# Kernel optimization log

Measured on AMD Instinct MI355X. Metric: run time of the kernel, lower is better.

The kernel has to match this reference:

```python
import jax, jax.numpy as jnp
import numpy as np

B, N, M = 2, 2048, 2048
D = 1024          # query_dim == context_dim == inner_dim
H, DH = 16, 64    # heads, dim_head
SCALE = DH ** -0.5


def setup_inputs() -> dict:
    key = jax.random.key(0)
    ks = jax.random.split(key, 7)
    s = 0.02
    return {
        "x": jax.random.normal(ks[0], (B, N, D), jnp.float32),
        "context": jax.random.normal(ks[1], (B, M, D), jnp.float32),
        "Wq": jax.random.normal(ks[2], (D, H * DH), jnp.float32) * s,
        "Wk": jax.random.normal(ks[3], (D, H * DH), jnp.float32) * s,
        "Wv": jax.random.normal(ks[4], (D, H * DH), jnp.float32) * s,
        "Wo": jax.random.normal(ks[5], (H * DH, D), jnp.float32) * s,
        "bo": jax.random.normal(ks[6], (D,), jnp.float32) * s,
    }


def reference(x, context, Wq, Wk, Wv, Wo, bo):
    # Linear projections (bias-free, as in to_q/to_k/to_v)
    q = (x @ Wq).reshape(B, N, H, DH)        # [B,N,H,DH]
    k = (context @ Wk).reshape(B, M, H, DH)  # [B,M,H,DH]
    v = (context @ Wv).reshape(B, M, H, DH)
    # QK^T * scale, softmax over keys, then AV
    sim = jnp.einsum('bnhd,bmhd->bhnm', q, k) * SCALE  # [B,H,N,M]
    attn = jax.nn.softmax(sim, axis=-1)
    out = jnp.einsum('bhnm,bmhd->bnhd', attn, v)       # [B,N,H,DH]
    out = out.reshape(B, N, H * DH)
    return out @ Wo + bo  # to_out Linear; dropout=0 is identity
```

## Files before the change

kernel.cpp:

```cpp
#include <hip/hip_runtime.h>

#define B_  2
#define N_  2048
#define M_  2048
#define D_  1024
#define H_  16
#define DH_ 64

typedef __bf16 bf16x8 __attribute__((ext_vector_type(8)));
typedef __bf16 bf16x4 __attribute__((ext_vector_type(4)));
typedef short  short4v __attribute__((ext_vector_type(4)));
typedef float  f32x4  __attribute__((ext_vector_type(4)));

#define GAS(p) ((__attribute__((address_space(1))) void*)(p))
#define LAS(p) ((__attribute__((address_space(3))) void*)(p))

#define QPRESCALE 0.18033688011112042f

__device__ __forceinline__ unsigned short f2bf(float f) {
    unsigned int u = __builtin_bit_cast(unsigned int, f);
    u += 0x7fffu + ((u >> 16) & 1u);
    return (unsigned short)(u >> 16);
}

__global__ __launch_bounds__(256) void prep(
    const float* __restrict__ x, const float* __restrict__ ctx,
    const float* __restrict__ Wq, const float* __restrict__ Wk,
    const float* __restrict__ Wv, const float* __restrict__ Wo,
    unsigned short* __restrict__ xb, unsigned short* __restrict__ cb,
    unsigned short* __restrict__ WTbase)
{
    if (blockIdx.z == 4) {
        int blk = blockIdx.y * 32 + blockIdx.x;
        int stride = 1024 * 256;
        for (int i = blk * 256 + threadIdx.x; i < 2097152; i += stride) {
            const float4* src; unsigned short* dst; int j;
            if (i < 1048576) { src = (const float4*)x;   dst = xb; j = i; }
            else             { src = (const float4*)ctx; dst = cb; j = i - 1048576; }
            float4 v = src[j];
            ushort4 o = make_ushort4(f2bf(v.x), f2bf(v.y), f2bf(v.z), f2bf(v.w));
            *(ushort4*)(dst + 4*j) = o;
        }
        return;
    }
    const float* W = (blockIdx.z == 0) ? Wq : (blockIdx.z == 1) ? Wk
                    : (blockIdx.z == 2) ? Wv : Wo;
    unsigned short* WT = WTbase + (size_t)blockIdx.z * 1048576;
    __shared__ unsigned short t[32][33];
    int tx = threadIdx.x & 31, ty8 = threadIdx.x >> 5;
    int c = blockIdx.x * 32 + tx;
#pragma unroll
    for (int i = 0; i < 4; ++i) {
        int r = blockIdx.y * 32 + i*8 + ty8;
        t[i*8 + ty8][tx] = f2bf(W[(size_t)r * 1024 + c]);
    }
    __syncthreads();
    int c2 = blockIdx.y * 32 + tx;
#pragma unroll
    for (int i = 0; i < 4; ++i) {
        int r2 = blockIdx.x * 32 + i*8 + ty8;
        WT[(size_t)r2 * 1024 + c2] = t[tx][i*8 + ty8];
    }
}

__global__ __launch_bounds__(256) void gemm128(
    const unsigned short* __restrict__ xb,
    const unsigned short* __restrict__ cb,
    const unsigned short* __restrict__ wT,
    const unsigned short* __restrict__ aoA,
    unsigned short* __restrict__ qkv_out,
    const float* __restrict__ bo,
    float* __restrict__ outF,
    int base_mode)
{
    __shared__ __align__(16) unsigned short As[128*32];
    __shared__ __align__(16) unsigned short Bs[128*32];

    const int mode = base_mode + blockIdx.z;
    const unsigned short* Amat;
    const unsigned short* Bt;
    if (mode == 0)      { Amat = wT;               Bt = xb; }
    else if (mode == 1) { Amat = wT + 1048576;     Bt = cb; }
    else if (mode == 2) { Amat = cb;               Bt = wT + 2*1048576; }
    else                { Amat = wT + 3*1048576;   Bt = aoA; }

    const int tid = threadIdx.x;
    const int w = tid >> 6, l = tid & 63;
    const int quad = l >> 4, l16 = l & 15;
    const int wm = w & 1, wn = w >> 1;
    int row0, col0;
    if (mode == 2) { row0 = blockIdx.x * 128; col0 = blockIdx.y * 128; }
    else           { row0 = blockIdx.y * 128; col0 = blockIdx.x * 128; }

    f32x4 acc[4][4];
#pragma unroll
    for (int i = 0; i < 4; ++i)
#pragma unroll
        for (int j = 0; j < 4; ++j) acc[i][j] = (f32x4){0.f, 0.f, 0.f, 0.f};

    for (int k0 = 0; k0 < 1024; k0 += 32) {
        __syncthreads();
#pragma unroll
        for (int i = 0; i < 2; ++i) {
            int s = i*256 + w*64 + l;
            int m = s >> 2, c = s & 3;
            int cs = c ^ ((m >> 1) & 3);
            __builtin_amdgcn_global_load_lds(
                GAS(Amat + (size_t)(row0 + m)*1024 + k0 + cs*8),
                LAS(As + (i*256 + w*64)*8), 16, 0, 0);
            __builtin_amdgcn_global_load_lds(
                GAS(Bt + (size_t)(col0 + m)*1024 + k0 + cs*8),
                LAS(Bs + (i*256 + w*64)*8), 16, 0, 0);
        }
        __syncthreads();

        bf16x8 af[4], bfr[4];
#pragma unroll
        for (int mt = 0; mt < 4; ++mt) {
            int m = wm*64 + mt*16 + l16;
            af[mt] = *reinterpret_cast<const bf16x8*>(As + m*32 + (quad ^ ((m >> 1) & 3))*8);
            int n = wn*64 + mt*16 + l16;
            bfr[mt] = *reinterpret_cast<const bf16x8*>(Bs + n*32 + (quad ^ ((n >> 1) & 3))*8);
        }
#pragma unroll
        for (int mt = 0; mt < 4; ++mt)
#pragma unroll
            for (int nt = 0; nt < 4; ++nt)
                acc[mt][nt] = __builtin_amdgcn_mfma_f32_16x16x32_bf16(
                    af[mt], bfr[nt], acc[mt][nt], 0, 0, 0);
    }

    if (mode == 3) {
#pragma unroll
        for (int mt = 0; mt < 4; ++mt) {
            int c = row0 + wm*64 + mt*16 + quad*4;
            float4 bv = *(const float4*)(bo + c);
#pragma unroll
            for (int nt = 0; nt < 4; ++nt) {
                int n = col0 + wn*64 + nt*16 + l16;
                float4 ov = make_float4(acc[mt][nt][0] + bv.x, acc[mt][nt][1] + bv.y,
                                        acc[mt][nt][2] + bv.z, acc[mt][nt][3] + bv.w);
                *(float4*)(outF + (size_t)n*1024 + c) = ov;
            }
        }
    } else if (mode == 2) {
#pragma unroll
        for (int mt = 0; mt < 4; ++mt) {
            int gr = row0 + wm*64 + mt*16 + quad*4;
            int b = gr >> 11, nidx = gr & 2047;
#pragma unroll
            for (int nt = 0; nt < 4; ++nt) {
                int col = col0 + wn*64 + nt*16 + l16;
                int h = col >> 6, d = col & 63;
                ushort4 pk = make_ushort4(f2bf(acc[mt][nt][0]), f2bf(acc[mt][nt][1]),
                                          f2bf(acc[mt][nt][2]), f2bf(acc[mt][nt][3]));
                *(ushort4*)(qkv_out + (size_t)2*4194304
                            + (size_t)((b*16 + h)*64 + d)*2048 + nidx) = pk;
            }
        }
    } else {
        const float qs = (mode == 0) ? QPRESCALE : 1.0f;
        unsigned short* obase = qkv_out + (size_t)mode*4194304;
#pragma unroll
        for (int nt = 0; nt < 4; ++nt) {
            int n = col0 + wn*64 + nt*16 + l16;
            int b = n >> 11, nidx = n & 2047;
#pragma unroll
            for (int mt = 0; mt < 4; ++mt) {
                int c = row0 + wm*64 + mt*16 + quad*4;
                int h = c >> 6, d = c & 63;
                ushort4 pkv = make_ushort4(
                    f2bf(acc[mt][nt][0] * qs), f2bf(acc[mt][nt][1] * qs),
                    f2bf(acc[mt][nt][2] * qs), f2bf(acc[mt][nt][3] * qs));
                *(ushort4*)(obase + (size_t)((b*16 + h)*2048 + nidx)*64 + d) = pkv;
            }
        }
    }
}

__global__ __launch_bounds__(256, 2) void flash_attn(
    const unsigned short* __restrict__ qw,
    const unsigned short* __restrict__ kw,
    const unsigned short* __restrict__ vtw,
    unsigned short* __restrict__ ao)
{
    __shared__ __align__(16) unsigned short Tile[2][9216];

    const int tid = threadIdx.x;
    const int w = tid >> 6, l = tid & 63;
    const int quad = l >> 4, l16 = l & 15;
    const int bh = blockIdx.z * H_ + blockIdx.y;
    const int q0 = blockIdx.x * 128 + w * 32;

    int goff[5];
#pragma unroll
    for (int i = 0; i < 5; ++i) {
        int n = i*256 + w*64 + l;
        int m = (n < 576) ? n : n - 576;
        int row = m / 9, c = m % 9;  if (c > 7) c = 7;
        goff[i] = (n < 576) ? row*64 + c*8 : row*2048 + c*8;
    }
    const unsigned short* kbase = kw + (size_t)bh*131072;
    const unsigned short* vbase = vtw + (size_t)bh*131072;

    bf16x8 qf[2][2];
#pragma unroll
    for (int qg = 0; qg < 2; ++qg)
#pragma unroll
        for (int s = 0; s < 2; ++s)
            qf[qg][s] = *reinterpret_cast<const bf16x8*>(
                qw + (size_t)(bh*2048 + q0 + qg*16 + l16)*64 + s*32 + quad*8);

    f32x4 accO[2][4];
#pragma unroll
    for (int qg = 0; qg < 2; ++qg)
#pragma unroll
        for (int td = 0; td < 4; ++td) accO[qg][td] = (f32x4){0.f, 0.f, 0.f, 0.f};
    float lpart[2] = {0.f, 0.f};

    const f32x4 zz = (f32x4){0.f, 0.f, 0.f, 0.f};

    {
#pragma unroll
        for (int i = 0; i < 4; ++i) {
            const unsigned short* bp = (i*4 + w < 9) ? kbase : vbase;
            __builtin_amdgcn_global_load_lds(GAS(bp + goff[i]),
                LAS(&Tile[0][(i*256 + w*64)*8]), 16, 0, 0);
        }
        if (w < 2)
            __builtin_amdgcn_global_load_lds(GAS(vbase + goff[4]),
                LAS(&Tile[0][(1024 + w*64)*8]), 16, 0, 0);
    }

    for (int it = 0; it < 32; ++it) {
        __syncthreads();
        const int cur = it & 1;

        if (it + 1 < 32) {
            const unsigned short* kp = kbase + (it+1)*4096;
            const unsigned short* vp = vbase + (it+1)*64;
#pragma unroll
            for (int i = 0; i < 4; ++i) {
                const unsigned short* bp = (i*4 + w < 9) ? kp : vp;
                __builtin_amdgcn_global_load_lds(GAS(bp + goff[i]),
                    LAS(&Tile[cur^1][(i*256 + w*64)*8]), 16, 0, 0);
            }
            if (w < 2)
                __builtin_amdgcn_global_load_lds(GAS(vp + goff[4]),
                    LAS(&Tile[cur^1][(1024 + w*64)*8]), 16, 0, 0);
        }

        const unsigned short* Ks = &Tile[cur][0];
        const unsigned short* Vs = &Tile[cur][4608];

        f32x4 sac[2][4];
#pragma unroll
        for (int t = 0; t < 4; ++t) {
            const unsigned short* krow = Ks + (t*16 + l16)*72 + quad*8;
            bf16x8 kf0 = *reinterpret_cast<const bf16x8*>(krow);
            bf16x8 kf1 = *reinterpret_cast<const bf16x8*>(krow + 32);
            sac[0][t] = __builtin_amdgcn_mfma_f32_16x16x32_bf16(kf0, qf[0][0], zz, 0, 0, 0);
            sac[1][t] = __builtin_amdgcn_mfma_f32_16x16x32_bf16(kf0, qf[1][0], zz, 0, 0, 0);
            sac[0][t] = __builtin_amdgcn_mfma_f32_16x16x32_bf16(kf1, qf[0][1], sac[0][t], 0, 0, 0);
            sac[1][t] = __builtin_amdgcn_mfma_f32_16x16x32_bf16(kf1, qf[1][1], sac[1][t], 0, 0, 0);
        }

        short4v pk[2][4];
#pragma unroll
        for (int qg = 0; qg < 2; ++qg) {
            float s0 = 0.f, s1 = 0.f, s2 = 0.f, s3 = 0.f;
#pragma unroll
            for (int t = 0; t < 4; ++t) {
                float p0 = __builtin_amdgcn_exp2f(sac[qg][t][0]);
                float p1 = __builtin_amdgcn_exp2f(sac[qg][t][1]);
                float p2 = __builtin_amdgcn_exp2f(sac[qg][t][2]);
                float p3 = __builtin_amdgcn_exp2f(sac[qg][t][3]);
                s0 += p0; s1 += p1; s2 += p2; s3 += p3;
                bf16x4 pb;
                pb[0] = (__bf16)p0; pb[1] = (__bf16)p1;
                pb[2] = (__bf16)p2; pb[3] = (__bf16)p3;
                pk[qg][t] = __builtin_bit_cast(short4v, pb);
            }
            lpart[qg] += (s0 + s1) + (s2 + s3);
        }

#pragma unroll
        for (int td = 0; td < 4; ++td) {
            const unsigned short* vrow = Vs + (td*16 + l16)*72 + quad*4;
#pragma unroll
            for (int t = 0; t < 4; ++t) {
                short4v vf = *reinterpret_cast<const short4v*>(vrow + t*16);
                accO[0][td] = __builtin_amdgcn_mfma_f32_16x16x16bf16_1k(
                    vf, pk[0][t], accO[0][td], 0, 0, 0);
                accO[1][td] = __builtin_amdgcn_mfma_f32_16x16x16bf16_1k(
                    vf, pk[1][t], accO[1][td], 0, 0, 0);
            }
        }
    }

#pragma unroll
    for (int qg = 0; qg < 2; ++qg) {
        float s = lpart[qg];
        s += __shfl_xor(s, 16);
        s += __shfl_xor(s, 32);
        float inv = 1.f / s;
        const size_t rowbase =
            (size_t)(blockIdx.z*2048 + q0 + qg*16 + l16)*1024 + blockIdx.y*64;
#pragma unroll
        for (int td = 0; td < 4; ++td)
#pragma unroll
            for (int r = 0; r < 4; ++r)
                ao[rowbase + td*16 + quad*4 + r] = f2bf(accO[qg][td][r] * inv);
    }
}

extern "C" void kernel_launch(void* const* d_in, const int* in_sizes, int n_in,
                              void* d_out, int out_size, void* d_ws, size_t ws_size,
                              hipStream_t stream)
{
    const float* x   = (const float*)d_in[0];
    const float* ctx = (const float*)d_in[1];
    const float* Wq  = (const float*)d_in[2];
    const float* Wk  = (const float*)d_in[3];
    const float* Wv  = (const float*)d_in[4];
    const float* Wo  = (const float*)d_in[5];
    const float* bo  = (const float*)d_in[6];
    float* out = (float*)d_out;

    unsigned short* ws  = (unsigned short*)d_ws;
    unsigned short* xb  = ws;
    unsigned short* cb  = ws + 4194304;
    unsigned short* wT  = ws + 8388608;
    unsigned short* qkv = ws + 12582912;
    unsigned short* ao  = ws;

    prep<<<dim3(32, 32, 5), dim3(256), 0, stream>>>(x, ctx, Wq, Wk, Wv, Wo, xb, cb, wT);
    gemm128<<<dim3(32, 8, 3), dim3(256), 0, stream>>>(xb, cb, wT, ao, qkv, bo, out, 0);
    flash_attn<<<dim3(16, 16, 2), dim3(256), 0, stream>>>(qkv, qkv + 4194304, qkv + 8388608, ao);
    gemm128<<<dim3(32, 8, 1), dim3(256), 0, stream>>>(xb, cb, wT, ao, qkv, bo, out, 3);
}
```

Before: 209.7 us.

## Use 16x16x32 MFMA for PV with permlane-swapped packed P and setprio

Packs the exponentiated scores with v_cvt_pk_bf16_f32 and reorders them across lanes with permlane32/16 swaps. This lets the P·V product use the K=32 bf16 MFMA with 8-wide V fragment loads, halving the MFMA and LDS-load instruction count. It also raises wave priority around the MFMA sections so they interleave better with other waves' softmax work. The cost is the added permlane shuffles, and correctness depends on the lane permutation matching the new V fragment layout.

```diff
diff --git a/kernel.cpp b/kernel.cpp
--- a/kernel.cpp
+++ b/kernel.cpp
@@ -11,6 +11,7 @@
 typedef __bf16 bf16x4 __attribute__((ext_vector_type(4)));
 typedef short  short4v __attribute__((ext_vector_type(4)));
 typedef float  f32x4  __attribute__((ext_vector_type(4)));
+typedef unsigned int u32x4v __attribute__((ext_vector_type(4)));
 
 #define GAS(p) ((__attribute__((address_space(1))) void*)(p))
 #define LAS(p) ((__attribute__((address_space(3))) void*)(p))
@@ -21,6 +22,12 @@
     unsigned int u = __builtin_bit_cast(unsigned int, f);
     u += 0x7fffu + ((u >> 16) & 1u);
     return (unsigned short)(u >> 16);
+}
+
+__device__ __forceinline__ unsigned cvtpkbf(float a, float b) {
+    unsigned r;
+    asm("v_cvt_pk_bf16_f32 %0, %1, %2" : "=v"(r) : "v"(a), "v"(b));
+    return r;
 }
 
 __global__ __launch_bounds__(256) void prep(
@@ -254,6 +261,7 @@
         const unsigned short* Vs = &Tile[cur][4608];
 
         f32x4 sac[2][4];
+        __builtin_amdgcn_s_setprio(1);
 #pragma unroll
         for (int t = 0; t < 4; ++t) {
             const unsigned short* krow = Ks + (t*16 + l16)*72 + quad*8;
@@ -264,38 +272,49 @@
             sac[0][t] = __builtin_amdgcn_mfma_f32_16x16x32_bf16(kf1, qf[0][1], sac[0][t], 0, 0, 0);
             sac[1][t] = __builtin_amdgcn_mfma_f32_16x16x32_bf16(kf1, qf[1][1], sac[1][t], 0, 0, 0);
         }
-
-        short4v pk[2][4];
+        __builtin_amdgcn_s_setprio(0);
+
+        u32x4v pB[2][2];
 #pragma unroll
         for (int qg = 0; qg < 2; ++qg) {
             float s0 = 0.f, s1 = 0.f, s2 = 0.f, s3 = 0.f;
 #pragma unroll
-            for (int t = 0; t < 4; ++t) {
-                float p0 = __builtin_amdgcn_exp2f(sac[qg][t][0]);
-                float p1 = __builtin_amdgcn_exp2f(sac[qg][t][1]);
-                float p2 = __builtin_amdgcn_exp2f(sac[qg][t][2]);
-                float p3 = __builtin_amdgcn_exp2f(sac[qg][t][3]);
-                s0 += p0; s1 += p1; s2 += p2; s3 += p3;
-                bf16x4 pb;
-                pb[0] = (__bf16)p0; pb[1] = (__bf16)p1;
-                pb[2] = (__bf16)p2; pb[3] = (__bf16)p3;
-                pk[qg][t] = __builtin_bit_cast(short4v, pb);
+            for (int t2 = 0; t2 < 2; ++t2) {
+                float pe0 = __builtin_amdgcn_exp2f(sac[qg][2*t2][0]);
+                float pe1 = __builtin_amdgcn_exp2f(sac[qg][2*t2][1]);
+                float pe2 = __builtin_amdgcn_exp2f(sac[qg][2*t2][2]);
+                float pe3 = __builtin_amdgcn_exp2f(sac[qg][2*t2][3]);
+                float po0 = __builtin_amdgcn_exp2f(sac[qg][2*t2+1][0]);
+                float po1 = __builtin_amdgcn_exp2f(sac[qg][2*t2+1][1]);
+                float po2 = __builtin_amdgcn_exp2f(sac[qg][2*t2+1][2]);
+                float po3 = __builtin_amdgcn_exp2f(sac[qg][2*t2+1][3]);
+                s0 += pe0 + po0; s1 += pe1 + po1;
+                s2 += pe2 + po2; s3 += pe3 + po3;
+                unsigned b0 = cvtpkbf(pe0, pe1), b1 = cvtpkbf(pe2, pe3);
+                unsigned b2 = cvtpkbf(po0, po1), b3 = cvtpkbf(po2, po3);
+                asm("v_permlane32_swap_b32 %0, %1" : "+v"(b0), "+v"(b2));
+                asm("v_permlane16_swap_b32 %0, %1" : "+v"(b0), "+v"(b2));
+                asm("v_permlane32_swap_b32 %0, %1" : "+v"(b1), "+v"(b3));
+                asm("v_permlane16_swap_b32 %0, %1" : "+v"(b1), "+v"(b3));
+                pB[qg][t2] = (u32x4v){b0, b1, b2, b3};
             }
             lpart[qg] += (s0 + s1) + (s2 + s3);
         }
 
+        __builtin_amdgcn_s_setprio(1);
 #pragma unroll
         for (int td = 0; td < 4; ++td) {
-            const unsigned short* vrow = Vs + (td*16 + l16)*72 + quad*4;
-#pragma unroll
-            for (int t = 0; t < 4; ++t) {
-                short4v vf = *reinterpret_cast<const short4v*>(vrow + t*16);
-                accO[0][td] = __builtin_amdgcn_mfma_f32_16x16x16bf16_1k(
-                    vf, pk[0][t], accO[0][td], 0, 0, 0);
-                accO[1][td] = __builtin_amdgcn_mfma_f32_16x16x16bf16_1k(
-                    vf, pk[1][t], accO[1][td], 0, 0, 0);
-            }
-        }
+            const unsigned short* vrow = Vs + (td*16 + l16)*72 + quad*8;
+#pragma unroll
+            for (int t2 = 0; t2 < 2; ++t2) {
+                bf16x8 vf = *reinterpret_cast<const bf16x8*>(vrow + t2*32);
+                accO[0][td] = __builtin_amdgcn_mfma_f32_16x16x32_bf16(
+                    vf, __builtin_bit_cast(bf16x8, pB[0][t2]), accO[0][td], 0, 0, 0);
+                accO[1][td] = __builtin_amdgcn_mfma_f32_16x16x32_bf16(
+                    vf, __builtin_bit_cast(bf16x8, pB[1][t2]), accO[1][td], 0, 0, 0);
+            }
+        }
+        __builtin_amdgcn_s_setprio(0);
     }
 
 #pragma unroll
```

Result: faster. 203.9 us (-2.7%).
